# Performance work log

Hardware: AMD Instinct MI355X
Metric: run time of the kernel (lower is better)

Reference implementation:

```python
import jax, jax.numpy as jnp
import numpy as np

B, R, H, Q, D = 16, 400, 8, 64, 1200  # BatchSize, ROIs, heads, q, BOLDs
THRESH_INIT = 0.01

def setup_inputs() -> dict:
    key = jax.random.key(0)
    k1, k2, k3, k4, k5 = jax.random.split(key, 5)
    s = 1.0 / np.sqrt(D)
    return {
        "x": jax.random.normal(k1, (B, R, D), dtype=jnp.float32),
        "Wq": jax.random.normal(k2, (D, H * Q), dtype=jnp.float32) * s,
        "bq": jax.random.normal(k3, (H * Q,), dtype=jnp.float32) * 0.01,
        "Wk": jax.random.normal(k4, (D, H * Q), dtype=jnp.float32) * s,
        "bk": jax.random.normal(k5, (H * Q,), dtype=jnp.float32) * 0.01,
        "threshold": jnp.ones((), dtype=jnp.float32),
    }

def reference(x, Wq, bq, Wk, bk, threshold):
    # Q,K projections: [B,R,H*Q] -> [B,R,H,Q]
    q = (x @ Wq + bq).reshape(B, R, H, Q)
    k = (x @ Wk + bk).reshape(B, R, H, Q)
    # QK^T per head: [B,H,R,R]
    rel = jnp.einsum("bihq,bjhq->bhij", q, k) / jnp.float32(Q)
    rel = jax.nn.softmax(rel, axis=-1)
    # threshold-subtract + relu sparsification (learned scalar, init 0.01)
    rel = jax.nn.relu(rel - threshold * THRESH_INIT)
    return rel
```

## Files before the change

### kernel.cpp

```cpp
#include <hip/hip_runtime.h>
#include <stdint.h>

#define DPAD 1216
#define MROWS 6400

typedef float f32x4 __attribute__((ext_vector_type(4)));
typedef __bf16 bf16x8 __attribute__((ext_vector_type(8)));
typedef __attribute__((address_space(3))) uint8_t as3_u8;
typedef __attribute__((address_space(1))) uint8_t as1_u8;

__device__ __forceinline__ void gload_lds16(const void* g, void* l) {
  __builtin_amdgcn_global_load_lds((as1_u8*)g, (as3_u8*)l, 16, 0, 0);
}

__global__ void cvt_x(const float* __restrict__ x, __bf16* __restrict__ xb) {
  const int id = blockIdx.x * 256 + threadIdx.x;
  const int row = id / 152;
  const int c = id - row * 152;
  const int col = c * 8;
  bf16x8 v;
  if (col < 1200) {
    const float4* p = (const float4*)(x + row * 1200 + col);
    const float4 f0 = p[0], f1 = p[1];
    v[0] = (__bf16)f0.x; v[1] = (__bf16)f0.y; v[2] = (__bf16)f0.z; v[3] = (__bf16)f0.w;
    v[4] = (__bf16)f1.x; v[5] = (__bf16)f1.y; v[6] = (__bf16)f1.z; v[7] = (__bf16)f1.w;
  } else {
#pragma unroll
    for (int i = 0; i < 8; ++i) v[i] = (__bf16)0.0f;
  }
  *(bf16x8*)(xb + (size_t)row * DPAD + col) = v;
}

__global__ void cvt_w(const float* __restrict__ wq, const float* __restrict__ wk,
                      __bf16* __restrict__ wt) {
  const int id = blockIdx.x * 256 + threadIdx.x;
  const int n = id / 152;
  const int c = id - n * 152;
  const int k0 = c * 8;
  const float* src = (n < 512) ? (wq + n) : (wk + (n - 512));
  bf16x8 v;
#pragma unroll
  for (int i = 0; i < 8; ++i) {
    const int k = k0 + i;
    v[i] = (k < 1200) ? (__bf16)src[(size_t)k * 512] : (__bf16)0.0f;
  }
  *(bf16x8*)(wt + (size_t)n * DPAD + k0) = v;
}

__global__ __launch_bounds__(256) void gemm_qk(const __bf16* __restrict__ xb,
                                               const __bf16* __restrict__ wt,
                                               const float* __restrict__ bq,
                                               const float* __restrict__ bk,
                                               __bf16* __restrict__ qk) {
  __shared__ __bf16 As[128 * 32];
  __shared__ __bf16 Bs[128 * 32];
  const int bid = blockIdx.x;
  const int wg = (bid & 7) * 50 + (bid >> 3);
  const int n0 = (wg / 50) * 128;
  const int m0 = (wg % 50) * 128;
  const int t = threadIdx.x;
  const int lane = t & 63;
  const int wid = t >> 6;
  const int wr = wid >> 1, wc = wid & 1;
  const int lrow = lane & 15, lk = lane >> 4;

  f32x4 acc[4][4];
#pragma unroll
  for (int i = 0; i < 4; ++i)
#pragma unroll
    for (int j = 0; j < 4; ++j) acc[i][j] = (f32x4){0.f, 0.f, 0.f, 0.f};

  for (int k0 = 0; k0 < DPAD; k0 += 32) {
#pragma unroll
    for (int it = 0; it < 2; ++it) {
      const int id = it * 256 + t;
      const int row = id >> 2, cc = id & 3;
      gload_lds16(xb + (size_t)(m0 + row) * DPAD + k0 + cc * 8, (char*)As + id * 16);
      gload_lds16(wt + (size_t)(n0 + row) * DPAD + k0 + cc * 8, (char*)Bs + id * 16);
    }
    __syncthreads();
    bf16x8 a[4], bfr[4];
#pragma unroll
    for (int i = 0; i < 4; ++i)
      a[i] = *(const bf16x8*)(As + (wr * 64 + i * 16 + lrow) * 32 + lk * 8);
#pragma unroll
    for (int i = 0; i < 4; ++i)
      bfr[i] = *(const bf16x8*)(Bs + (wc * 64 + i * 16 + lrow) * 32 + lk * 8);
#pragma unroll
    for (int mi = 0; mi < 4; ++mi)
#pragma unroll
      for (int ni = 0; ni < 4; ++ni)
        acc[mi][ni] = __builtin_amdgcn_mfma_f32_16x16x32_bf16(a[mi], bfr[ni], acc[mi][ni], 0, 0, 0);
    __syncthreads();
  }
#pragma unroll
  for (int mi = 0; mi < 4; ++mi) {
#pragma unroll
    for (int ni = 0; ni < 4; ++ni) {
      const int gr0 = m0 + wr * 64 + mi * 16 + lk * 4;
      const int gc = n0 + wc * 64 + ni * 16 + lrow;
      const float bias = (gc < 512) ? bq[gc] : bk[gc - 512];
#pragma unroll
      for (int r = 0; r < 4; ++r)
        qk[(size_t)(gr0 + r) * 1024 + gc] = (__bf16)(acc[mi][ni][r] + bias);
    }
  }
}

__global__ __launch_bounds__(256) void attn(const __bf16* __restrict__ qk,
                                            const float* __restrict__ thr_p,
                                            float* __restrict__ out) {
  __shared__ float slds[16 * 400];
  const int bh = blockIdx.y;
  const int b = bh >> 3;
  const int h = bh & 7;
  const int r0 = blockIdx.x * 16;
  const int t = threadIdx.x;
  const int lane = t & 63;
  const int wid = t >> 6;
  const int lrow = lane & 15, lk = lane >> 4;
  const __bf16* kbase = qk + (size_t)(b * 400) * 1024 + 512 + h * 64;
  const __bf16* qbase = qk + (size_t)(b * 400 + r0) * 1024 + h * 64;

  bf16x8 aq[2];
#pragma unroll
  for (int kk = 0; kk < 2; ++kk)
    aq[kk] = *(const bf16x8*)(qbase + (size_t)lrow * 1024 + kk * 32 + lk * 8);

  for (int jt = wid; jt < 25; jt += 4) {
    f32x4 acc = (f32x4){0.f, 0.f, 0.f, 0.f};
#pragma unroll
    for (int kk = 0; kk < 2; ++kk) {
      const bf16x8 bkf = *(const bf16x8*)(kbase + (size_t)(jt * 16 + lrow) * 1024 + kk * 32 + lk * 8);
      acc = __builtin_amdgcn_mfma_f32_16x16x32_bf16(aq[kk], bkf, acc, 0, 0, 0);
    }
    const int scol = jt * 16 + lrow;
#pragma unroll
    for (int r = 0; r < 4; ++r)
      slds[(lk * 4 + r) * 400 + scol] = acc[r] * 0.015625f;
  }
  __syncthreads();

  const int row = t >> 4, c = t & 15;
  const float thr = thr_p[0] * 0.01f;
  float vals[25];
  float m = -1e30f;
#pragma unroll
  for (int j = 0; j < 25; ++j) {
    vals[j] = slds[row * 400 + j * 16 + c];
    m = fmaxf(m, vals[j]);
  }
#pragma unroll
  for (int off = 8; off >= 1; off >>= 1) m = fmaxf(m, __shfl_xor(m, off, 16));
  float sum = 0.f;
#pragma unroll
  for (int j = 0; j < 25; ++j) {
    vals[j] = __expf(vals[j] - m);
    sum += vals[j];
  }
#pragma unroll
  for (int off = 8; off >= 1; off >>= 1) sum += __shfl_xor(sum, off, 16);
  const float inv = 1.0f / sum;
  float* orow = out + ((size_t)bh * 400 + r0 + row) * 400;
#pragma unroll
  for (int j = 0; j < 25; ++j) {
    const float p = vals[j] * inv - thr;
    orow[j * 16 + c] = p > 0.f ? p : 0.f;
  }
}

extern "C" void kernel_launch(void* const* d_in, const int* in_sizes, int n_in,
                              void* d_out, int out_size, void* d_ws, size_t ws_size,
                              hipStream_t stream) {
  const float* x   = (const float*)d_in[0];
  const float* Wq  = (const float*)d_in[1];
  const float* bq  = (const float*)d_in[2];
  const float* Wk  = (const float*)d_in[3];
  const float* bk  = (const float*)d_in[4];
  const float* thr = (const float*)d_in[5];
  char* ws = (char*)d_ws;
  __bf16* xb = (__bf16*)ws;
  __bf16* wt = (__bf16*)(ws + 15564800);
  __bf16* qk = (__bf16*)(ws + 18055168);
  float* out = (float*)d_out;

  cvt_x<<<dim3(3800), dim3(256), 0, stream>>>(x, xb);
  cvt_w<<<dim3(608), dim3(256), 0, stream>>>(Wq, Wk, wt);
  gemm_qk<<<dim3(400), dim3(256), 0, stream>>>(xb, wt, bq, bk, qk);
  attn<<<dim3(25, 128), dim3(256), 0, stream>>>(qk, thr, out);
}
```

Baseline: 81.93 us.

## Fuse conversion and projection GEMM into one cooperative kernel with grid sync

```diff
diff --git a/kernel.cpp b/kernel.cpp
--- a/kernel.cpp
+++ b/kernel.cpp
@@ -1,8 +1,10 @@
 #include <hip/hip_runtime.h>
+#include <hip/hip_cooperative_groups.h>
 #include <stdint.h>
 
 #define DPAD 1216
-#define MROWS 6400
+#define N_CVT 4408
+#define NB_COOP 768
 
 typedef float f32x4 __attribute__((ext_vector_type(4)));
 typedef __bf16 bf16x8 __attribute__((ext_vector_type(8)));
@@ -13,38 +15,118 @@
   __builtin_amdgcn_global_load_lds((as1_u8*)g, (as3_u8*)l, 16, 0, 0);
 }
 
-__global__ void cvt_x(const float* __restrict__ x, __bf16* __restrict__ xb) {
-  const int id = blockIdx.x * 256 + threadIdx.x;
-  const int row = id / 152;
-  const int c = id - row * 152;
-  const int col = c * 8;
-  bf16x8 v;
-  if (col < 1200) {
-    const float4* p = (const float4*)(x + row * 1200 + col);
-    const float4 f0 = p[0], f1 = p[1];
-    v[0] = (__bf16)f0.x; v[1] = (__bf16)f0.y; v[2] = (__bf16)f0.z; v[3] = (__bf16)f0.w;
-    v[4] = (__bf16)f1.x; v[5] = (__bf16)f1.y; v[6] = (__bf16)f1.z; v[7] = (__bf16)f1.w;
+__device__ __forceinline__ void do_cvt_unit(int u, int t,
+    const float* __restrict__ x, const float* __restrict__ wq,
+    const float* __restrict__ wk, __bf16* __restrict__ xb,
+    __bf16* __restrict__ wt) {
+  if (u < 3800) {
+    const int id = u * 256 + t;
+    const int row = id / 152;
+    const int c = id - row * 152;
+    const int col = c * 8;
+    bf16x8 v;
+    if (col < 1200) {
+      const float4* p = (const float4*)(x + row * 1200 + col);
+      const float4 f0 = p[0], f1 = p[1];
+      v[0] = (__bf16)f0.x; v[1] = (__bf16)f0.y; v[2] = (__bf16)f0.z; v[3] = (__bf16)f0.w;
+      v[4] = (__bf16)f1.x; v[5] = (__bf16)f1.y; v[6] = (__bf16)f1.z; v[7] = (__bf16)f1.w;
+    } else {
+#pragma unroll
+      for (int i = 0; i < 8; ++i) v[i] = (__bf16)0.0f;
+    }
+    *(bf16x8*)(xb + (size_t)row * DPAD + col) = v;
   } else {
-#pragma unroll
-    for (int i = 0; i < 8; ++i) v[i] = (__bf16)0.0f;
-  }
-  *(bf16x8*)(xb + (size_t)row * DPAD + col) = v;
-}
-
-__global__ void cvt_w(const float* __restrict__ wq, const float* __restrict__ wk,
-                      __bf16* __restrict__ wt) {
-  const int id = blockIdx.x * 256 + threadIdx.x;
-  const int n = id / 152;
-  const int c = id - n * 152;
-  const int k0 = c * 8;
-  const float* src = (n < 512) ? (wq + n) : (wk + (n - 512));
-  bf16x8 v;
-#pragma unroll
-  for (int i = 0; i < 8; ++i) {
-    const int k = k0 + i;
-    v[i] = (k < 1200) ? (__bf16)src[(size_t)k * 512] : (__bf16)0.0f;
-  }
-  *(bf16x8*)(wt + (size_t)n * DPAD + k0) = v;
+    const int id = (u - 3800) * 256 + t;
+    const int n = id / 152;
+    const int c = id - n * 152;
+    const int k0 = c * 8;
+    const float* src = (n < 512) ? (wq + n) : (wk + (n - 512));
+    bf16x8 v;
+#pragma unroll
+    for (int i = 0; i < 8; ++i) {
+      const int k = k0 + i;
+      v[i] = (k < 1200) ? (__bf16)src[(size_t)k * 512] : (__bf16)0.0f;
+    }
+    *(bf16x8*)(wt + (size_t)n * DPAD + k0) = v;
+  }
+}
+
+__device__ __forceinline__ void do_gemm_tile(int m0, int n0, int t,
+    const __bf16* __restrict__ xb, const __bf16* __restrict__ wt,
+    const float* __restrict__ bq, const float* __restrict__ bk,
+    __bf16* __restrict__ qk, __bf16* As, __bf16* Bs) {
+  const int lane = t & 63;
+  const int wid = t >> 6;
+  const int wr = wid >> 1, wc = wid & 1;
+  const int lrow = lane & 15, lk = lane >> 4;
+
+  f32x4 acc[4][4];
+#pragma unroll
+  for (int i = 0; i < 4; ++i)
+#pragma unroll
+    for (int j = 0; j < 4; ++j) acc[i][j] = (f32x4){0.f, 0.f, 0.f, 0.f};
+
+  for (int k0 = 0; k0 < DPAD; k0 += 32) {
+#pragma unroll
+    for (int it = 0; it < 2; ++it) {
+      const int id = it * 256 + t;
+      const int row = id >> 2, cc = id & 3;
+      gload_lds16(xb + (size_t)(m0 + row) * DPAD + k0 + cc * 8, (char*)As + id * 16);
+      gload_lds16(wt + (size_t)(n0 + row) * DPAD + k0 + cc * 8, (char*)Bs + id * 16);
+    }
+    __syncthreads();
+    bf16x8 a[4], bfr[4];
+#pragma unroll
+    for (int i = 0; i < 4; ++i)
+      a[i] = *(const bf16x8*)(As + (wr * 64 + i * 16 + lrow) * 32 + lk * 8);
+#pragma unroll
+    for (int i = 0; i < 4; ++i)
+      bfr[i] = *(const bf16x8*)(Bs + (wc * 64 + i * 16 + lrow) * 32 + lk * 8);
+#pragma unroll
+    for (int mi = 0; mi < 4; ++mi)
+#pragma unroll
+      for (int ni = 0; ni < 4; ++ni)
+        acc[mi][ni] = __builtin_amdgcn_mfma_f32_16x16x32_bf16(a[mi], bfr[ni], acc[mi][ni], 0, 0, 0);
+    __syncthreads();
+  }
+#pragma unroll
+  for (int mi = 0; mi < 4; ++mi) {
+#pragma unroll
+    for (int ni = 0; ni < 4; ++ni) {
+      const int gr0 = m0 + wr * 64 + mi * 16 + lk * 4;
+      const int gc = n0 + wc * 64 + ni * 16 + lrow;
+      const float bias = (gc < 512) ? bq[gc] : bk[gc - 512];
+#pragma unroll
+      for (int r = 0; r < 4; ++r)
+        qk[(size_t)(gr0 + r) * 1024 + gc] = (__bf16)(acc[mi][ni][r] + bias);
+    }
+  }
+}
+
+__global__ __launch_bounds__(256, 3) void front_coop(
+    const float* __restrict__ x,  const float* __restrict__ wq,
+    const float* __restrict__ bq, const float* __restrict__ wk,
+    const float* __restrict__ bk, __bf16* __restrict__ xb,
+    __bf16* __restrict__ wt, __bf16* __restrict__ qk) {
+  __shared__ __bf16 As[128 * 32];
+  __shared__ __bf16 Bs[128 * 32];
+  const int t = threadIdx.x;
+
+  for (int u = blockIdx.x; u < N_CVT; u += gridDim.x)
+    do_cvt_unit(u, t, x, wq, wk, xb, wt);
+
+  cooperative_groups::this_grid().sync();
+
+  const int b = blockIdx.x;
+  const int tt = (b * 25 + 47) / 48;
+  if (tt < 400 && (tt * 48) / 25 == b)
+    do_gemm_tile((tt >> 3) * 128, (tt & 7) * 128, t, xb, wt, bq, bk, qk, As, Bs);
+}
+
+__global__ void cvt_fused(const float* __restrict__ x,
+                          const float* __restrict__ wq, const float* __restrict__ wk,
+                          __bf16* __restrict__ xb, __bf16* __restrict__ wt) {
+  do_cvt_unit(blockIdx.x, threadIdx.x, x, wq, wk, xb, wt);
 }
 
 __global__ __launch_bounds__(256) void gemm_qk(const __bf16* __restrict__ xb,
@@ -58,53 +140,7 @@
   const int wg = (bid & 7) * 50 + (bid >> 3);
   const int n0 = (wg / 50) * 128;
   const int m0 = (wg % 50) * 128;
-  const int t = threadIdx.x;
-  const int lane = t & 63;
-  const int wid = t >> 6;
-  const int wr = wid >> 1, wc = wid & 1;
-  const int lrow = lane & 15, lk = lane >> 4;
-
-  f32x4 acc[4][4];
-#pragma unroll
-  for (int i = 0; i < 4; ++i)
-#pragma unroll
-    for (int j = 0; j < 4; ++j) acc[i][j] = (f32x4){0.f, 0.f, 0.f, 0.f};
-
-  for (int k0 = 0; k0 < DPAD; k0 += 32) {
-#pragma unroll
-    for (int it = 0; it < 2; ++it) {
-      const int id = it * 256 + t;
-      const int row = id >> 2, cc = id & 3;
-      gload_lds16(xb + (size_t)(m0 + row) * DPAD + k0 + cc * 8, (char*)As + id * 16);
-      gload_lds16(wt + (size_t)(n0 + row) * DPAD + k0 + cc * 8, (char*)Bs + id * 16);
-    }
-    __syncthreads();
-    bf16x8 a[4], bfr[4];
-#pragma unroll
-    for (int i = 0; i < 4; ++i)
-      a[i] = *(const bf16x8*)(As + (wr * 64 + i * 16 + lrow) * 32 + lk * 8);
-#pragma unroll
-    for (int i = 0; i < 4; ++i)
-      bfr[i] = *(const bf16x8*)(Bs + (wc * 64 + i * 16 + lrow) * 32 + lk * 8);
-#pragma unroll
-    for (int mi = 0; mi < 4; ++mi)
-#pragma unroll
-      for (int ni = 0; ni < 4; ++ni)
-        acc[mi][ni] = __builtin_amdgcn_mfma_f32_16x16x32_bf16(a[mi], bfr[ni], acc[mi][ni], 0, 0, 0);
-    __syncthreads();
-  }
-#pragma unroll
-  for (int mi = 0; mi < 4; ++mi) {
-#pragma unroll
-    for (int ni = 0; ni < 4; ++ni) {
-      const int gr0 = m0 + wr * 64 + mi * 16 + lk * 4;
-      const int gc = n0 + wc * 64 + ni * 16 + lrow;
-      const float bias = (gc < 512) ? bq[gc] : bk[gc - 512];
-#pragma unroll
-      for (int r = 0; r < 4; ++r)
-        qk[(size_t)(gr0 + r) * 1024 + gc] = (__bf16)(acc[mi][ni][r] + bias);
-    }
-  }
+  do_gemm_tile(m0, n0, threadIdx.x, xb, wt, bq, bk, qk, As, Bs);
 }
 
 __global__ __launch_bounds__(256) void attn(const __bf16* __restrict__ qk,
@@ -184,8 +220,14 @@
   __bf16* qk = (__bf16*)(ws + 18055168);
   float* out = (float*)d_out;
 
-  cvt_x<<<dim3(3800), dim3(256), 0, stream>>>(x, xb);
-  cvt_w<<<dim3(608), dim3(256), 0, stream>>>(Wq, Wk, wt);
-  gemm_qk<<<dim3(400), dim3(256), 0, stream>>>(xb, wt, bq, bk, qk);
+  void* kargs[] = {(void*)&x, (void*)&Wq, (void*)&bq, (void*)&Wk, (void*)&bk,
+                   (void*)&xb, (void*)&wt, (void*)&qk};
+  hipError_t e = hipLaunchCooperativeKernel((const void*)front_coop,
+                                            dim3(NB_COOP), dim3(256),
+                                            kargs, 0, stream);
+  if (e != hipSuccess) {
+    cvt_fused<<<dim3(N_CVT), dim3(256), 0, stream>>>(x, Wq, Wk, xb, wt);
+    gemm_qk<<<dim3(400), dim3(256), 0, stream>>>(xb, wt, bq, bk, qk);
+  }
   attn<<<dim3(25, 128), dim3(256), 0, stream>>>(qk, thr, out);
 }
```

Result: slower. 179.0 us (+118.4%).
